# Kernel optimization log

Measured on AMD Instinct MI355X. Metric: run time of the kernel, lower is better.

Reference implementation:

```python
import jax, jax.numpy as jnp
import numpy as np

HIDDEN = 2048
NUM_HEADS = 16
HEAD_DIM = HIDDEN // NUM_HEADS


def setup_inputs() -> dict:
    key = jax.random.key(0)
    ks = jax.random.split(key, 10)
    B, S = 2, 2048
    scale = 1.0 / np.sqrt(HIDDEN)
    inp = {
        "x": jax.random.normal(ks[0], (B, S, HIDDEN), dtype=jnp.float32),
        "attention_mask": jnp.zeros((B, S), dtype=jnp.float32),
        "Wq": jax.random.normal(ks[1], (HIDDEN, HIDDEN), dtype=jnp.float32) * scale,
        "bq": jnp.zeros((HIDDEN,), dtype=jnp.float32),
        "Wk": jax.random.normal(ks[2], (HIDDEN, HIDDEN), dtype=jnp.float32) * scale,
        "bk": jnp.zeros((HIDDEN,), dtype=jnp.float32),
        "Wv": jax.random.normal(ks[3], (HIDDEN, HIDDEN), dtype=jnp.float32) * scale,
        "bv": jnp.zeros((HIDDEN,), dtype=jnp.float32),
        "Wo": jax.random.normal(ks[4], (HIDDEN, HIDDEN), dtype=jnp.float32) * scale,
        "bo": jnp.zeros((HIDDEN,), dtype=jnp.float32),
    }
    return inp


def _split_heads(t):
    # [B, S, H*D] -> [B, H, S, D]
    B, S, _ = t.shape
    return t.reshape(B, S, NUM_HEADS, HEAD_DIM).transpose(0, 2, 1, 3)


def reference(x, attention_mask, Wq, bq, Wk, bk, Wv, bv, Wo, bo):
    B, S, _ = x.shape
    # Linear layers: y = x @ W^T + b (torch nn.Linear convention)
    q = _split_heads(x @ Wq.T + bq)  # [B, H, S, D]
    k = _split_heads(x @ Wk.T + bk)
    v = _split_heads(x @ Wv.T + bv)
    scale = 1.0 / jnp.sqrt(jnp.asarray(HEAD_DIM, dtype=x.dtype))
    scores = jnp.einsum("bhqd,bhkd->bhqk", q, k) * scale  # [B, H, S, S]
    scores = scores + attention_mask[:, None, None, :]  # additive mask broadcast
    attn = jax.nn.softmax(scores, axis=-1)
    out = jnp.einsum("bhqk,bhkd->bhqd", attn, v)  # [B, H, S, D]
    out = out.transpose(0, 2, 1, 3).reshape(B, S, HIDDEN)
    return out @ Wo.T + bo
```

## Files before the change

### kernel.cpp

```cpp
#include <hip/hip_runtime.h>
#include <math.h>

constexpr int S_LEN = 2048;
constexpr int HID   = 2048;
constexpr int NH    = 16;
constexpr int HD    = 128;

typedef __attribute__((ext_vector_type(8))) short short8;
typedef __attribute__((ext_vector_type(4))) float floatx4;

static __device__ __forceinline__ ushort f2bf(float f) {
  union { float f; unsigned u; } v; v.f = f;
  unsigned r = (v.u + 0x7fffu + ((v.u >> 16) & 1u)) >> 16;
  return (ushort)r;
}
static __device__ __forceinline__ ushort f2bf_fast(float f) {
  union { float f; unsigned u; } v; v.f = f;
  return (ushort)((v.u + 0x8000u) >> 16);
}

static __device__ __forceinline__ void glds16(const ushort* g, ushort* l) {
  __builtin_amdgcn_global_load_lds(
      (const __attribute__((address_space(1))) void*)g,
      (__attribute__((address_space(3))) void*)l, 16, 0, 0);
}

static __device__ __forceinline__ void barrier_raw() {
  __builtin_amdgcn_s_barrier();
  asm volatile("" ::: "memory");
}

static __device__ __forceinline__ void cvt4(ushort* dst, const float* src, size_t i) {
  const float4 v = ((const float4*)src)[i];
  ushort4 u = {f2bf(v.x), f2bf(v.y), f2bf(v.z), f2bf(v.w)};
  ((ushort4*)dst)[i] = u;
}

__global__ __launch_bounds__(256)
void convert_all(const float* __restrict__ x,
                 const float* __restrict__ wq, const float* __restrict__ wk,
                 const float* __restrict__ wv, const float* __restrict__ wo,
                 ushort* __restrict__ xb, ushort* __restrict__ wqb,
                 ushort* __restrict__ wkb, ushort* __restrict__ wvb,
                 ushort* __restrict__ wob) {
  const size_t gid = blockIdx.x * 256 + threadIdx.x;
  const size_t T = gridDim.x * 256;
  const size_t NX = (size_t)4096 * HID / 4;
  const size_t NW = (size_t)HID * HID / 4;
  for (size_t i = gid; i < NX; i += T) cvt4(xb, x, i);
  for (size_t i = gid; i < NW; i += T) {
    cvt4(wqb, wq, i);
    cvt4(wkb, wk, i);
    cvt4(wvb, wv, i);
    cvt4(wob, wo, i);
  }
}

#define MFMA_QUAD(MH, NH_)                                                    \
  __builtin_amdgcn_s_setprio(1);                                              \
  _Pragma("unroll")                                                           \
  for (int kc = 0; kc < 2; ++kc) {                                            \
    _Pragma("unroll")                                                         \
    for (int mi = 0; mi < 2; ++mi) {                                          \
      _Pragma("unroll")                                                       \
      for (int ni = 0; ni < 2; ++ni) {                                        \
        acc[2*(MH)+mi][2*(NH_)+ni] = __builtin_amdgcn_mfma_f32_16x16x32_bf16( \
            af[kc][2*(MH)+mi], bf[kc][2*(NH_)+ni], acc[2*(MH)+mi][2*(NH_)+ni],\
            0, 0, 0);                                                         \
      }                                                                       \
    }                                                                         \
  }                                                                           \
  __builtin_amdgcn_s_setprio(0);

template <bool BF16OUT>
__device__ __forceinline__
void gemm8_core(const ushort* __restrict__ A, const ushort* __restrict__ W,
                const float* __restrict__ bias, void* __restrict__ Cv,
                int m0, int n0) {
  __shared__ __align__(16) ushort lds[49152];
  constexpr int NT = HID / 64;

  const int tid  = threadIdx.x;
  const int lane = tid & 63;
  const int w    = tid >> 6;
  const int wm   = w >> 1, wn = w & 1;
  const int n16  = lane & 15, q4 = lane >> 4;
  const int n7   = n16 & 7;

  const int srow  = lane >> 3;
  const int sslot = lane & 7;
  const int sl    = sslot ^ srow;

  const ushort* asrc[4];
  const ushort* bsrc[2];
  #pragma unroll
  for (int c = 0; c < 4; ++c)
    asrc[c] = A + (size_t)(m0 + c*64 + w*8 + srow) * HID + sl*8;
  #pragma unroll
  for (int c = 0; c < 2; ++c)
    bsrc[c] = W + (size_t)(n0 + c*64 + w*8 + srow) * HID + sl*8;

  ushort* const A0 = lds;
  ushort* const A1 = lds + 16384;
  ushort* const B0 = lds + 32768;
  ushort* const B1 = lds + 40960;
  const int wofs = w * 512;

  floatx4 acc[4][4];
  #pragma unroll
  for (int i = 0; i < 4; ++i)
    #pragma unroll
    for (int j = 0; j < 4; ++j) acc[i][j] = (floatx4)0.f;

  #pragma unroll
  for (int c = 0; c < 4; ++c) glds16(asrc[c], A0 + c*4096 + wofs);
  #pragma unroll
  for (int c = 0; c < 2; ++c) glds16(bsrc[c], B0 + c*4096 + wofs);
  #pragma unroll
  for (int c = 0; c < 4; ++c) glds16(asrc[c] + 64, A1 + c*4096 + wofs);
  asm volatile("s_waitcnt vmcnt(4)" ::: "memory");
  barrier_raw();

  for (int t = 0; t < NT; ++t) {
    const ushort* cA = (t & 1) ? A1 : A0;
    const ushort* cB = (t & 1) ? B1 : B0;
    ushort* nB = (t & 1) ? B0 : B1;
    ushort* rA = (t & 1) ? A1 : A0;

    if (t + 1 < NT) {
      glds16(bsrc[0] + (size_t)(t+1)*64, nB + wofs);
      glds16(bsrc[1] + (size_t)(t+1)*64, nB + 4096 + wofs);
    }
    short8 af[2][4], bf[2][4];
    #pragma unroll
    for (int kc = 0; kc < 2; ++kc) {
      #pragma unroll
      for (int mt = 0; mt < 4; ++mt)
        af[kc][mt] = *(const short8*)(cA + (wm*64 + mt*16 + n16)*64
                                         + (((kc*4 + q4) ^ n7) * 8));
      #pragma unroll
      for (int nt = 0; nt < 4; ++nt)
        bf[kc][nt] = *(const short8*)(cB + (wn*64 + nt*16 + n16)*64
                                         + (((kc*4 + q4) ^ n7) * 8));
    }
    barrier_raw();
    asm volatile("s_waitcnt lgkmcnt(0)" ::: "memory");
    __builtin_amdgcn_sched_barrier(0);
    MFMA_QUAD(0, 0)
    barrier_raw();

    const bool st2 = (t + 2 < NT);
    if (st2) {
      glds16(asrc[0] + (size_t)(t+2)*64, rA + 0*4096 + wofs);
      glds16(asrc[1] + (size_t)(t+2)*64, rA + 1*4096 + wofs);
    }
    MFMA_QUAD(0, 1)
    barrier_raw();

    if (st2) {
      glds16(asrc[2] + (size_t)(t+2)*64, rA + 2*4096 + wofs);
      glds16(asrc[3] + (size_t)(t+2)*64, rA + 3*4096 + wofs);
    }
    MFMA_QUAD(1, 0)
    barrier_raw();

    MFMA_QUAD(1, 1)
    if (st2) asm volatile("s_waitcnt vmcnt(4)" ::: "memory");
    else     asm volatile("s_waitcnt vmcnt(0)" ::: "memory");
    barrier_raw();
  }

  float bv4[4];
  #pragma unroll
  for (int nt = 0; nt < 4; ++nt) bv4[nt] = bias[n0 + wn*64 + nt*16 + n16];
  #pragma unroll
  for (int mt = 0; mt < 4; ++mt)
    #pragma unroll
    for (int nt = 0; nt < 4; ++nt)
      #pragma unroll
      for (int r = 0; r < 4; ++r) {
        const int row = m0 + wm*64 + mt*16 + q4*4 + r;
        const int col = n0 + wn*64 + nt*16 + n16;
        if (BF16OUT)
          ((ushort*)Cv)[(size_t)row * HID + col] = f2bf(acc[mt][nt][r] + bv4[nt]);
        else
          ((float*)Cv)[(size_t)row * HID + col] = acc[mt][nt][r] + bv4[nt];
      }
}

static __device__ __forceinline__ void tile_coords(int& m0, int& n0) {
  const int id = blockIdx.y * gridDim.x + blockIdx.x;
  const int s  = ((id & 7) << 5) | (id >> 3);
  m0 = (s >> 4) * 256;
  n0 = (s & 15) * 128;
}

__global__ __launch_bounds__(512, 2)
void gemm_qkv(const ushort* __restrict__ xb,
              const ushort* __restrict__ wqb, const ushort* __restrict__ wkb,
              const ushort* __restrict__ wvb,
              const float* __restrict__ bq, const float* __restrict__ bk,
              const float* __restrict__ bv,
              ushort* __restrict__ qb, ushort* __restrict__ kb_, ushort* __restrict__ vb) {
  const ushort* W; const float* bias; ushort* C;
  if (blockIdx.z == 0)      { W = wqb; bias = bq; C = qb;  }
  else if (blockIdx.z == 1) { W = wkb; bias = bk; C = kb_; }
  else                      { W = wvb; bias = bv; C = vb;  }
  int m0, n0; tile_coords(m0, n0);
  gemm8_core<true>(xb, W, bias, C, m0, n0);
}

__global__ __launch_bounds__(512, 2)
void gemm_o(const ushort* __restrict__ ao, const ushort* __restrict__ wob,
            const float* __restrict__ bo, float* __restrict__ out) {
  int m0, n0; tile_coords(m0, n0);
  gemm8_core<false>(ao, wob, bo, out, m0, n0);
}

__global__ __launch_bounds__(256)
void transpose_v(const ushort* __restrict__ vb, ushort* __restrict__ vt) {
  __shared__ ushort T[64][72];
  const int t  = threadIdx.x;
  const int bh = blockIdx.z;
  const int b = bh >> 4, h = bh & 15;
  const int s0 = blockIdx.x * 64;
  const int d0 = blockIdx.y * 64;
  {
    const int r = t >> 2, c = (t & 3) * 16;
    const ushort* src = vb + (size_t)(b*S_LEN + s0 + r)*HID + h*HD + d0 + c;
    *(uint4*)&T[r][c]     = *(const uint4*)src;
    *(uint4*)&T[r][c + 8] = *(const uint4*)(src + 8);
  }
  __syncthreads();
  {
    const int dd = t >> 2, c = (t & 3) * 16;
    ushort tmp[16];
    #pragma unroll
    for (int j = 0; j < 16; ++j) tmp[j] = T[c + j][dd];
    ushort* dst = vt + (size_t)((b*NH + h)*HD + d0 + dd)*S_LEN + s0 + c;
    *(uint4*)dst       = *(uint4*)tmp;
    *(uint4*)(dst + 8) = *(uint4*)(tmp + 8);
  }
}

__global__ __launch_bounds__(256, 2)
void attn_mfma(const ushort* __restrict__ qb, const ushort* __restrict__ kbuf,
               const ushort* __restrict__ vtb, const float* __restrict__ mask,
               ushort* __restrict__ ao) {
  __shared__ __align__(16) ushort SM[25600];

  const int tid  = threadIdx.x;
  const int w    = tid >> 6;
  const int lane = tid & 63;
  const int n16  = lane & 15;
  const int q4   = lane >> 4;
  const int n7   = n16 & 7;
  const int b  = blockIdx.y >> 4;
  const int h  = blockIdx.y & 15;
  const int q0 = blockIdx.x * 128;
  const float scale = 0.08838834764831845f;

  ushort* Ks = SM;
  ushort* Vs = SM + 8192;
  ushort* Pw = SM + 16384 + w * 2304;

  short8 aq[2][4];
  #pragma unroll
  for (int mt = 0; mt < 2; ++mt) {
    const ushort* qrow = qb + (size_t)(b*S_LEN + q0 + w*32 + mt*16 + n16)*HID + h*HD;
    #pragma unroll
    for (int kc = 0; kc < 4; ++kc)
      aq[mt][kc] = *(const short8*)(qrow + kc*32 + q4*8);
  }

  const ushort* ksrc[4];
  const ushort* vsrc[4];
  #pragma unroll
  for (int i = 0; i < 4; ++i) {
    const int p = (w*4 + i)*64 + lane;
    { const int rho = p >> 4, pc = p & 15;
      const int cl = (pc & 8) | ((pc ^ rho) & 7);
      ksrc[i] = kbuf + (size_t)(b*S_LEN + rho)*HID + h*HD + cl*8; }
    { const int rho = p >> 3, pc = p & 7;
      const int cl = (pc ^ rho) & 7;
      vsrc[i] = vtb + ((size_t)(b*NH + h)*HD + rho)*S_LEN + cl*8; }
  }

  floatx4 oacc[2][8];
  float lp[2][4];
  #pragma unroll
  for (int mt = 0; mt < 2; ++mt) {
    #pragma unroll
    for (int dt = 0; dt < 8; ++dt) oacc[mt][dt] = (floatx4)0.f;
    #pragma unroll
    for (int r = 0; r < 4; ++r) lp[mt][r] = 0.f;
  }

  for (int kb0 = 0; kb0 < S_LEN; kb0 += 64) {
    __syncthreads();
    #pragma unroll
    for (int i = 0; i < 4; ++i) {
      glds16(ksrc[i] + (size_t)kb0 * HID, Ks + (w*4 + i)*512);
      glds16(vsrc[i] + kb0,               Vs + (w*4 + i)*512);
    }
    __syncthreads();

    floatx4 acc[2][4];
    #pragma unroll
    for (int mt = 0; mt < 2; ++mt)
      #pragma unroll
      for (int nt = 0; nt < 4; ++nt) acc[mt][nt] = (floatx4)0.f;
    #pragma unroll
    for (int nt = 0; nt < 4; ++nt) {
      #pragma unroll
      for (int kc = 0; kc < 4; ++kc) {
        const int cl = kc*4 + q4;
        const int pc = (cl & 8) | ((cl ^ n7) & 7);
        const short8 bk = *(const short8*)&Ks[(nt*16 + n16)*128 + pc*8];
        acc[0][nt] = __builtin_amdgcn_mfma_f32_16x16x32_bf16(aq[0][kc], bk, acc[0][nt], 0, 0, 0);
        acc[1][nt] = __builtin_amdgcn_mfma_f32_16x16x32_bf16(aq[1][kc], bk, acc[1][nt], 0, 0, 0);
      }
    }

    float mk[4];
    #pragma unroll
    for (int nt = 0; nt < 4; ++nt)
      mk[nt] = mask[(size_t)b*S_LEN + kb0 + nt*16 + n16];

    #pragma unroll
    for (int mt = 0; mt < 2; ++mt)
      #pragma unroll
      for (int r = 0; r < 4; ++r) {
        float p[4];
        #pragma unroll
        for (int nt = 0; nt < 4; ++nt) p[nt] = __expf(acc[mt][nt][r] * scale + mk[nt]);
        lp[mt][r] += (p[0] + p[1]) + (p[2] + p[3]);
        #pragma unroll
        for (int nt = 0; nt < 4; ++nt)
          Pw[(mt*16 + q4*4 + r)*72 + nt*16 + n16] = f2bf_fast(p[nt]);
      }

    #pragma unroll
    for (int kc2 = 0; kc2 < 2; ++kc2) {
      const short8 ap0 = *(const short8*)&Pw[(0*16 + n16)*72 + kc2*32 + q4*8];
      const short8 ap1 = *(const short8*)&Pw[(1*16 + n16)*72 + kc2*32 + q4*8];
      const int clb = kc2*4 + q4;
      const int pcb = (clb ^ n7) & 7;
      #pragma unroll
      for (int dt = 0; dt < 8; ++dt) {
        const short8 bvf = *(const short8*)&Vs[(dt*16 + n16)*64 + pcb*8];
        oacc[0][dt] = __builtin_amdgcn_mfma_f32_16x16x32_bf16(ap0, bvf, oacc[0][dt], 0, 0, 0);
        oacc[1][dt] = __builtin_amdgcn_mfma_f32_16x16x32_bf16(ap1, bvf, oacc[1][dt], 0, 0, 0);
      }
    }
  }

  #pragma unroll
  for (int mt = 0; mt < 2; ++mt)
    #pragma unroll
    for (int r = 0; r < 4; ++r) {
      float l = lp[mt][r];
      l += __shfl_xor(l, 1);
      l += __shfl_xor(l, 2);
      l += __shfl_xor(l, 4);
      l += __shfl_xor(l, 8);
      lp[mt][r] = 1.0f / l;
    }

  __syncthreads();
  ushort* dump = SM + w * 4352;
  #pragma unroll
  for (int mt = 0; mt < 2; ++mt)
    #pragma unroll
    for (int r = 0; r < 4; ++r) {
      const int row = mt*16 + q4*4 + r;
      #pragma unroll
      for (int dt = 0; dt < 8; ++dt)
        dump[row*136 + dt*16 + n16] = f2bf(oacc[mt][dt][r] * lp[mt][r]);
    }
  const int drow = lane >> 1, dhalf = lane & 1;
  const size_t gbase = (size_t)(b*S_LEN + q0 + w*32 + drow)*HID + h*HD + dhalf*64;
  #pragma unroll
  for (int j = 0; j < 8; ++j)
    *(uint4*)&ao[gbase + j*8] = *(const uint4*)&dump[drow*136 + dhalf*64 + j*8];
}

extern "C" void kernel_launch(void* const* d_in, const int* in_sizes, int n_in,
                              void* d_out, int out_size, void* d_ws, size_t ws_size,
                              hipStream_t stream) {
  (void)n_in; (void)out_size; (void)ws_size;
  const float* x    = (const float*)d_in[0];
  const float* mask = (const float*)d_in[1];
  const float* Wq   = (const float*)d_in[2];
  const float* bq   = (const float*)d_in[3];
  const float* Wk   = (const float*)d_in[4];
  const float* bk   = (const float*)d_in[5];
  const float* Wv   = (const float*)d_in[6];
  const float* bv   = (const float*)d_in[7];
  const float* Wo   = (const float*)d_in[8];
  const float* bo   = (const float*)d_in[9];
  float* out = (float*)d_out;

  const int B = in_sizes[0] / (S_LEN * HID);
  const int M = B * S_LEN;
  const size_t MH = (size_t)M * HID;
  const size_t WW = (size_t)HID * HID;

  ushort* xb   = (ushort*)d_ws;
  ushort* wqb  = xb   + MH;
  ushort* wkb  = wqb  + WW;
  ushort* wvb  = wkb  + WW;
  ushort* wob  = wvb  + WW;
  ushort* qb   = wob  + WW;
  ushort* kbuf = qb   + MH;
  ushort* vb   = kbuf + MH;
  ushort* vt   = vb   + MH;
  ushort* ao   = xb;

  convert_all<<<512, 256, 0, stream>>>(x, Wq, Wk, Wv, Wo, xb, wqb, wkb, wvb, wob);
  gemm_qkv<<<dim3(HID/128, M/256, 3), 512, 0, stream>>>(xb, wqb, wkb, wvb, bq, bk, bv, qb, kbuf, vb);
  transpose_v<<<dim3(S_LEN/64, HD/64, B*NH), 256, 0, stream>>>(vb, vt);
  attn_mfma<<<dim3(S_LEN/128, B*NH), 256, 0, stream>>>(qb, kbuf, vt, mask, ao);
  gemm_o<<<dim3(HID/128, M/256), 512, 0, stream>>>(ao, wob, bo, out);
}
```

Before: 403.1 us.

## Restructure GEMM prefetch schedule and overlap K/V loads in attention loop

The projection GEMM now stages whole A+B tiles two iterations ahead and splits each tile into two k-phases that each load fragments and run a full 4x4 MFMA block, replacing the interleaved quad-based scheduling. The attention kernel now issues the next K tile right after QK^T and the next V tile right after PV, using vmcnt waits instead of full syncthreads, so global-to-LDS loads overlap with softmax and MFMA work. It also adds setprio around the MFMA sections. The aim is to hide load latency and cut barrier stalls, at the cost of more barriers in the GEMM and a redundant reload of the last tile in attention.

```diff
diff --git a/kernel.cpp b/kernel.cpp
--- a/kernel.cpp
+++ b/kernel.cpp
@@ -56,21 +56,30 @@
   }
 }
 
-#define MFMA_QUAD(MH, NH_)                                                    \
-  __builtin_amdgcn_s_setprio(1);                                              \
-  _Pragma("unroll")                                                           \
-  for (int kc = 0; kc < 2; ++kc) {                                            \
+#define GEMM_PHASE(KC)                                                        \
+  {                                                                           \
+    short8 af[4], bf[4];                                                      \
     _Pragma("unroll")                                                         \
-    for (int mi = 0; mi < 2; ++mi) {                                          \
+    for (int mt = 0; mt < 4; ++mt)                                            \
+      af[mt] = *(const short8*)(cA + (wm*64 + mt*16 + n16)*64                 \
+                                   + ((((KC)*4 + q4) ^ n7) * 8));             \
+    _Pragma("unroll")                                                         \
+    for (int nt = 0; nt < 4; ++nt)                                            \
+      bf[nt] = *(const short8*)(cB + (wn*64 + nt*16 + n16)*64                 \
+                                   + ((((KC)*4 + q4) ^ n7) * 8));             \
+    barrier_raw();                                                            \
+    asm volatile("s_waitcnt lgkmcnt(0)" ::: "memory");                        \
+    __builtin_amdgcn_sched_barrier(0);                                        \
+    __builtin_amdgcn_s_setprio(1);                                            \
+    _Pragma("unroll")                                                         \
+    for (int mt = 0; mt < 4; ++mt)                                            \
       _Pragma("unroll")                                                       \
-      for (int ni = 0; ni < 2; ++ni) {                                        \
-        acc[2*(MH)+mi][2*(NH_)+ni] = __builtin_amdgcn_mfma_f32_16x16x32_bf16( \
-            af[kc][2*(MH)+mi], bf[kc][2*(NH_)+ni], acc[2*(MH)+mi][2*(NH_)+ni],\
-            0, 0, 0);                                                         \
-      }                                                                       \
-    }                                                                         \
-  }                                                                           \
-  __builtin_amdgcn_s_setprio(0);
+      for (int nt = 0; nt < 4; ++nt)                                          \
+        acc[mt][nt] = __builtin_amdgcn_mfma_f32_16x16x32_bf16(                \
+            af[mt], bf[nt], acc[mt][nt], 0, 0, 0);                            \
+    __builtin_amdgcn_s_setprio(0);                                            \
+    barrier_raw();                                                            \
+  }
 
 template <bool BF16OUT>
 __device__ __forceinline__
@@ -112,62 +121,33 @@
     #pragma unroll
     for (int j = 0; j < 4; ++j) acc[i][j] = (floatx4)0.f;
 
-  #pragma unroll
-  for (int c = 0; c < 4; ++c) glds16(asrc[c], A0 + c*4096 + wofs);
-  #pragma unroll
-  for (int c = 0; c < 2; ++c) glds16(bsrc[c], B0 + c*4096 + wofs);
-  #pragma unroll
-  for (int c = 0; c < 4; ++c) glds16(asrc[c] + 64, A1 + c*4096 + wofs);
-  asm volatile("s_waitcnt vmcnt(4)" ::: "memory");
+  auto stage_tile = [&](int t, ushort* Ab, ushort* Bb) {
+    #pragma unroll
+    for (int c = 0; c < 4; ++c) glds16(asrc[c] + (size_t)t*64, Ab + c*4096 + wofs);
+    #pragma unroll
+    for (int c = 0; c < 2; ++c) glds16(bsrc[c] + (size_t)t*64, Bb + c*4096 + wofs);
+  };
+
+  stage_tile(0, A0, B0);
+  stage_tile(1, A1, B1);
+  asm volatile("s_waitcnt vmcnt(6)" ::: "memory");
   barrier_raw();
 
   for (int t = 0; t < NT; ++t) {
     const ushort* cA = (t & 1) ? A1 : A0;
     const ushort* cB = (t & 1) ? B1 : B0;
-    ushort* nB = (t & 1) ? B0 : B1;
-    ushort* rA = (t & 1) ? A1 : A0;
-
-    if (t + 1 < NT) {
-      glds16(bsrc[0] + (size_t)(t+1)*64, nB + wofs);
-      glds16(bsrc[1] + (size_t)(t+1)*64, nB + 4096 + wofs);
+
+    GEMM_PHASE(0)
+    GEMM_PHASE(1)
+
+    if (t + 2 < NT) {
+      stage_tile(t + 2, (t & 1) ? A1 : A0, (t & 1) ? B1 : B0);
+      asm volatile("s_waitcnt vmcnt(6)" ::: "memory");
+      barrier_raw();
+    } else if (t + 1 < NT) {
+      asm volatile("s_waitcnt vmcnt(0)" ::: "memory");
+      barrier_raw();
     }
-    short8 af[2][4], bf[2][4];
-    #pragma unroll
-    for (int kc = 0; kc < 2; ++kc) {
-      #pragma unroll
-      for (int mt = 0; mt < 4; ++mt)
-        af[kc][mt] = *(const short8*)(cA + (wm*64 + mt*16 + n16)*64
-                                         + (((kc*4 + q4) ^ n7) * 8));
-      #pragma unroll
-      for (int nt = 0; nt < 4; ++nt)
-        bf[kc][nt] = *(const short8*)(cB + (wn*64 + nt*16 + n16)*64
-                                         + (((kc*4 + q4) ^ n7) * 8));
-    }
-    barrier_raw();
-    asm volatile("s_waitcnt lgkmcnt(0)" ::: "memory");
-    __builtin_amdgcn_sched_barrier(0);
-    MFMA_QUAD(0, 0)
-    barrier_raw();
-
-    const bool st2 = (t + 2 < NT);
-    if (st2) {
-      glds16(asrc[0] + (size_t)(t+2)*64, rA + 0*4096 + wofs);
-      glds16(asrc[1] + (size_t)(t+2)*64, rA + 1*4096 + wofs);
-    }
-    MFMA_QUAD(0, 1)
-    barrier_raw();
-
-    if (st2) {
-      glds16(asrc[2] + (size_t)(t+2)*64, rA + 2*4096 + wofs);
-      glds16(asrc[3] + (size_t)(t+2)*64, rA + 3*4096 + wofs);
-    }
-    MFMA_QUAD(1, 0)
-    barrier_raw();
-
-    MFMA_QUAD(1, 1)
-    if (st2) asm volatile("s_waitcnt vmcnt(4)" ::: "memory");
-    else     asm volatile("s_waitcnt vmcnt(0)" ::: "memory");
-    barrier_raw();
   }
 
   float bv4[4];
@@ -296,20 +276,28 @@
     for (int r = 0; r < 4; ++r) lp[mt][r] = 0.f;
   }
 
+  #pragma unroll
+  for (int i = 0; i < 4; ++i) glds16(ksrc[i], Ks + (w*4 + i)*512);
+  #pragma unroll
+  for (int i = 0; i < 4; ++i) glds16(vsrc[i], Vs + (w*4 + i)*512);
+
   for (int kb0 = 0; kb0 < S_LEN; kb0 += 64) {
-    __syncthreads();
-    #pragma unroll
-    for (int i = 0; i < 4; ++i) {
-      glds16(ksrc[i] + (size_t)kb0 * HID, Ks + (w*4 + i)*512);
-      glds16(vsrc[i] + kb0,               Vs + (w*4 + i)*512);
-    }
-    __syncthreads();
+    const int knext = (kb0 + 64 < S_LEN) ? kb0 + 64 : kb0;
+
+    asm volatile("s_waitcnt vmcnt(4)" ::: "memory");
+    barrier_raw();
+
+    float mk[4];
+    #pragma unroll
+    for (int nt = 0; nt < 4; ++nt)
+      mk[nt] = mask[(size_t)b*S_LEN + kb0 + nt*16 + n16];
 
     floatx4 acc[2][4];
     #pragma unroll
     for (int mt = 0; mt < 2; ++mt)
       #pragma unroll
       for (int nt = 0; nt < 4; ++nt) acc[mt][nt] = (floatx4)0.f;
+    __builtin_amdgcn_s_setprio(1);
     #pragma unroll
     for (int nt = 0; nt < 4; ++nt) {
       #pragma unroll
@@ -321,11 +309,12 @@
         acc[1][nt] = __builtin_amdgcn_mfma_f32_16x16x32_bf16(aq[1][kc], bk, acc[1][nt], 0, 0, 0);
       }
     }
-
-    float mk[4];
-    #pragma unroll
-    for (int nt = 0; nt < 4; ++nt)
-      mk[nt] = mask[(size_t)b*S_LEN + kb0 + nt*16 + n16];
+    __builtin_amdgcn_s_setprio(0);
+
+    barrier_raw();
+    #pragma unroll
+    for (int i = 0; i < 4; ++i)
+      glds16(ksrc[i] + (size_t)knext * HID, Ks + (w*4 + i)*512);
 
     #pragma unroll
     for (int mt = 0; mt < 2; ++mt)
@@ -340,6 +329,10 @@
           Pw[(mt*16 + q4*4 + r)*72 + nt*16 + n16] = f2bf_fast(p[nt]);
       }
 
+    asm volatile("s_waitcnt vmcnt(4)" ::: "memory");
+    barrier_raw();
+
+    __builtin_amdgcn_s_setprio(1);
     #pragma unroll
     for (int kc2 = 0; kc2 < 2; ++kc2) {
       const short8 ap0 = *(const short8*)&Pw[(0*16 + n16)*72 + kc2*32 + q4*8];
@@ -353,6 +346,12 @@
         oacc[1][dt] = __builtin_amdgcn_mfma_f32_16x16x32_bf16(ap1, bvf, oacc[1][dt], 0, 0, 0);
       }
     }
+    __builtin_amdgcn_s_setprio(0);
+
+    barrier_raw();
+    #pragma unroll
+    for (int i = 0; i < 4; ++i)
+      glds16(vsrc[i] + knext, Vs + (w*4 + i)*512);
   }
 
   #pragma unroll
```

Result: no change. 407.3 us (+1.0%).
